# Performance work log

Hardware: AMD Instinct MI355X
Metric: run time of the kernel (lower is better)

The kernel has to match this reference:

```python
import jax, jax.numpy as jnp
import numpy as np


def setup_inputs() -> dict:
    key = jax.random.key(0)
    k1, k2, k3, k4 = jax.random.split(key, 4)
    B, Tv, Ta, D = 8, 2048, 2048, 256
    return {
        "visual_features": jax.random.normal(k1, (B, Tv, D), dtype=jnp.float32),
        "audio_features": jax.random.normal(k2, (B, Ta, D), dtype=jnp.float32),
        "visual_weights": jax.random.uniform(k3, (D, D), dtype=jnp.float32),
        "audio_weights": jax.random.uniform(k4, (D, D), dtype=jnp.float32),
        "num_neighbors": 8,
    }


def _pairwise_l2(vm, am):
    # ||v - a|| via the expanded form to avoid the [B,Tv,Ta,D] intermediate.
    sq = (
        jnp.sum(vm * vm, -1)[:, :, None]
        + jnp.sum(am * am, -1)[:, None, :]
        - 2.0 * jnp.einsum("btd,bsd->bts", vm, am)
    )
    sq = jnp.maximum(sq, 0.0)
    # safe sqrt: subgradient 0 at 0 (matches torch.norm backward convention)
    return jnp.where(sq > 0, jnp.sqrt(jnp.where(sq > 0, sq, 1.0)), 0.0)


def reference(visual_features, audio_features, visual_weights, audio_weights, num_neighbors):
    vm = visual_features @ visual_weights  # [B,Tv,D]
    am = audio_features @ audio_weights    # [B,Ta,D]
    graph = jnp.exp(-_pairwise_l2(vm, am))  # [B,Tv,Ta]
    # topk over the visual axis (dim=1): move it last for lax.top_k
    _, idx = jax.lax.top_k(jnp.swapaxes(graph, 1, 2), num_neighbors)  # [B,Ta,k]
    idx = jnp.swapaxes(idx, 1, 2)  # [B,k,Ta]
    # broadcasted gather along axis 1: result [B,k,Ta,D]
    vn = jnp.take_along_axis(visual_features[:, :, None, :], idx[..., None], axis=1)
    an = jnp.take_along_axis(audio_features[:, :, None, :], idx[..., None], axis=1)
    # mean over dim=2 (the Ta axis of the gathered neighbors) -> [B,k,D]
    return vn.mean(axis=2), an.mean(axis=2)
```

## Files before the change

### kernel.cpp

```cpp
#include <hip/hip_runtime.h>
#include <cstddef>
#include <cstdint>

namespace {
constexpr int kB   = 8;
constexpr int kT   = 2048;
constexpr int kD   = 256;
constexpr int kK   = 8;
constexpr int kM   = kB * kT;
constexpr int kNCH = 64;
constexpr int kNC  = kB * kT;
constexpr int kColCap = 64;
constexpr int kOvCap  = 1 << 17;
constexpr int kStr = 264;
constexpr float kMinNormalF = 1.17549435e-38f;
}

typedef __attribute__((ext_vector_type(8)))  __bf16 bf16x8;
typedef __attribute__((ext_vector_type(16))) float  f32x16;

__device__ inline unsigned short f2bf_rne(float x) {
  unsigned u = __float_as_uint(x);
  unsigned r = (u + 0x7FFFu + ((u >> 16) & 1u)) >> 16;
  return (unsigned short)r;
}
__device__ inline float bf2f(unsigned short h) {
  return __uint_as_float((unsigned)h << 16);
}
union FragU { uint4 u4; bf16x8 v; };

__global__ __launch_bounds__(256) void prep(const float* __restrict__ W0,
                                            const float* __restrict__ W1,
                                            unsigned short* __restrict__ T0,
                                            unsigned short* __restrict__ T1,
                                            unsigned* __restrict__ zeroBase,
                                            int zeroWords) {
  const int blk = blockIdx.x;
  if (blk < 128) {
    const float* W = (blk & 64) ? W1 : W0;
    unsigned short* WT = (blk & 64) ? T1 : T0;
    const int t = blk & 63;
    const int c0 = (t & 7) * 32, k0 = (t >> 3) * 32;
    __shared__ float tile[32][33];
    const int tx = threadIdx.x & 31, ty = threadIdx.x >> 5;
#pragma unroll
    for (int i = 0; i < 4; ++i)
      tile[ty + i * 8][tx] = W[(size_t)(k0 + ty + i * 8) * kD + c0 + tx];
    __syncthreads();
#pragma unroll
    for (int i = 0; i < 4; ++i)
      WT[(size_t)(c0 + ty + i * 8) * kD + k0 + tx] = f2bf_rne(tile[tx][ty + i * 8]);
  } else {
    for (int i = (blk - 128) * 256 + threadIdx.x; i < zeroWords; i += 32 * 256)
      zeroBase[i] = 0u;
  }
}

__global__ __launch_bounds__(256) void gemm_hyb(const float* __restrict__ Xv,
                                                const float* __restrict__ Xa,
                                                const unsigned short* __restrict__ WvT,
                                                const unsigned short* __restrict__ WaT,
                                                unsigned short* __restrict__ Cv,
                                                unsigned short* __restrict__ Ca,
                                                float* __restrict__ nv,
                                                float* __restrict__ na) {
  __shared__ unsigned short S[64 * kStr];
  const int z = blockIdx.z;
  const float* X = z ? Xa : Xv;
  const unsigned short* WT = z ? WaT : WvT;
  unsigned short* Cb = z ? Ca : Cv;
  float* nrm = z ? na : nv;
  const int r0 = blockIdx.x * 64;
  const int cHalf = blockIdx.y;
  const int tid = threadIdx.x;
  const int w = tid >> 6, lane = tid & 63;
  const int wt = w & 1, wc = w >> 1;
  const int half = lane >> 5, ln = lane & 31;

#pragma unroll
  for (int i = 0; i < 16; ++i) {
    const int idx = i * 256 + tid;
    const int row = idx >> 6, g = idx & 63;
    const float4 v = *reinterpret_cast<const float4*>(X + (size_t)(r0 + row) * kD + g * 4);
    ushort4 o;
    o.x = f2bf_rne(v.x); o.y = f2bf_rne(v.y); o.z = f2bf_rne(v.z); o.w = f2bf_rne(v.w);
    *reinterpret_cast<ushort4*>(S + row * kStr + g * 4) = o;
  }
  __syncthreads();
  uint4 afr[16];
#pragma unroll
  for (int kc = 0; kc < 16; ++kc)
    afr[kc] = *reinterpret_cast<const uint4*>(S + (wt * 32 + ln) * kStr + kc * 16 + half * 8);

  float ns[16];
#pragma unroll
  for (int r = 0; r < 16; ++r) ns[r] = 0.0f;

  for (int ct = 0; ct < 2; ++ct) {
    const int c0 = (cHalf * 2 + ct) * 64;
    __syncthreads();
#pragma unroll
    for (int i = 0; i < 8; ++i) {
      const int idx = i * 256 + tid;
      const int row = idx >> 5, g = idx & 31;
      const uint4 v = *reinterpret_cast<const uint4*>(WT + (size_t)(c0 + row) * kD + g * 8);
      *reinterpret_cast<uint4*>(S + row * kStr + g * 8) = v;
    }
    __syncthreads();
    f32x16 acc;
#pragma unroll
    for (int i = 0; i < 16; ++i) acc[i] = 0.0f;
#pragma unroll
    for (int kc = 0; kc < 16; ++kc) {
      FragU fa, fb;
      fa.u4 = afr[kc];
      fb.u4 = *reinterpret_cast<const uint4*>(S + (wc * 32 + ln) * kStr + kc * 16 + half * 8);
      acc = __builtin_amdgcn_mfma_f32_32x32x16_bf16(fa.v, fb.v, acc, 0, 0, 0);
    }
    const int col = c0 + wc * 32 + ln;
#pragma unroll
    for (int r = 0; r < 16; ++r) {
      const int row = r0 + wt * 32 + (r & 3) + 8 * (r >> 2) + 4 * half;
      const unsigned short us = f2bf_rne(acc[r]);
      Cb[(size_t)row * kD + col] = us;
      const float f = bf2f(us);
      ns[r] += f * f;
    }
  }
#pragma unroll
  for (int r = 0; r < 16; ++r) {
    float v = ns[r];
#pragma unroll
    for (int off = 1; off < 32; off <<= 1) v += __shfl_xor(v, off, 64);
    if (ln == 0) {
      const int row = r0 + wt * 32 + (r & 3) + 8 * (r >> 2) + 4 * half;
      atomicAdd(nrm + row, v);
    }
  }
}

__global__ __launch_bounds__(256) void keys_v12(const unsigned short* __restrict__ vmb,
                                                const unsigned short* __restrict__ amb,
                                                const float* __restrict__ vn2,
                                                const float* __restrict__ an2,
                                                unsigned* __restrict__ colCount,
                                                uint2* __restrict__ colRecs,
                                                unsigned* __restrict__ ovCount,
                                                uint2* __restrict__ ovRecs) {
  __shared__ unsigned short S[64 * kStr];
  const int b = blockIdx.z;
  const int t0 = blockIdx.x * 128;
  const int sr0 = blockIdx.y * 256;
  const int tid = threadIdx.x;
  const int w = tid >> 6, lane = tid & 63;
  const int half = lane >> 5, ln = lane & 31;

  uint4 afr[16];
#pragma unroll
  for (int h = 0; h < 2; ++h) {
#pragma unroll
    for (int i = 0; i < 8; ++i) {
      const int idx = i * 256 + tid;
      const int row = idx >> 5, g = idx & 31;
      const uint4 v = *reinterpret_cast<const uint4*>(
          vmb + ((size_t)b * kT + t0 + h * 64 + row) * kD + g * 8);
      *reinterpret_cast<uint4*>(S + row * kStr + g * 8) = v;
    }
    __syncthreads();
    if ((w >> 1) == h) {
#pragma unroll
      for (int kc = 0; kc < 16; ++kc)
        afr[kc] = *reinterpret_cast<const uint4*>(S + ((w & 1) * 32 + ln) * kStr + kc * 16 + half * 8);
    }
    __syncthreads();
  }

  const float* v2p = vn2 + (size_t)b * kT + t0 + w * 32;

  for (int st = 0; st < 4; ++st) {
    const int s0 = sr0 + st * 64;
    if (st) __syncthreads();
#pragma unroll
    for (int i = 0; i < 8; ++i) {
      const int idx = i * 256 + tid;
      const int row = idx >> 5, g = idx & 31;
      const uint4 v = *reinterpret_cast<const uint4*>(
          amb + ((size_t)b * kT + s0 + row) * kD + g * 8);
      *reinterpret_cast<uint4*>(S + row * kStr + g * 8) = v;
    }
    __syncthreads();
    f32x16 acc[2];
#pragma unroll
    for (int j = 0; j < 2; ++j)
#pragma unroll
      for (int i = 0; i < 16; ++i) acc[j][i] = 0.0f;
#pragma unroll
    for (int kc = 0; kc < 16; ++kc) {
      FragU fa; fa.u4 = afr[kc];
#pragma unroll
      for (int ss = 0; ss < 2; ++ss) {
        FragU fb;
        fb.u4 = *reinterpret_cast<const uint4*>(S + (ss * 32 + ln) * kStr + kc * 16 + half * 8);
        acc[ss] = __builtin_amdgcn_mfma_f32_32x32x16_bf16(fa.v, fb.v, acc[ss], 0, 0, 0);
      }
    }
#pragma unroll
    for (int ss = 0; ss < 2; ++ss) {
      const int s = s0 + ss * 32 + ln;
      const float a2 = an2[(size_t)b * kT + s];
      const int c = (b << 11) | s;
#pragma unroll
      for (int g = 0; g < 4; ++g) {
        const float4 v2 = *reinterpret_cast<const float4*>(v2p + g * 8 + half * 4);
        const float v2a[4] = {v2.x, v2.y, v2.z, v2.w};
#pragma unroll
        for (int q = 0; q < 4; ++q) {
          const float raw = v2a[q] + a2 - 2.0f * acc[ss][4 * g + q];
          if (raw < 7744.0f) {
            const float dist = sqrtf(fmaxf(raw, 0.0f));
            const float e = expf(-dist);
            if (e >= kMinNormalF) {
              const int t = t0 + w * 32 + g * 8 + half * 4 + q;
              const unsigned slot = atomicAdd(&colCount[c], 1u);
              if (slot < (unsigned)kColCap) {
                colRecs[(size_t)c * kColCap + slot] = make_uint2(__float_as_uint(e), (unsigned)t);
              } else {
                const unsigned pos = ((unsigned)b << 22) | ((unsigned)s << 11) | (unsigned)t;
                const unsigned oi = atomicAdd(ovCount, 1u);
                if (oi < (unsigned)kOvCap) ovRecs[oi] = make_uint2(__float_as_uint(e), pos);
              }
            }
          }
        }
      }
    }
  }
}

__global__ __launch_bounds__(256) void finalize_topk(const unsigned* __restrict__ colCount,
                                                     const uint2* __restrict__ colRecs,
                                                     const unsigned* __restrict__ ovCount,
                                                     const uint2* __restrict__ ovRecs,
                                                     int* __restrict__ idxT) {
  const int c = blockIdx.x * 256 + threadIdx.x;
  unsigned K[8];
  int T[8];
#pragma unroll
  for (int i = 0; i < 8; ++i) { K[i] = 0u; T[i] = 0x7FFFFFFF; }
  const int cnt = (int)colCount[c];
  const int m = min(cnt, kColCap);
  for (int i = 0; i < m; ++i) {
    const uint2 r = colRecs[(size_t)c * kColCap + i];
    const unsigned kx = r.x;
    const int tx = (int)r.y;
    if (kx > K[7] || (kx == K[7] && tx < T[7])) {
      K[7] = kx; T[7] = tx;
#pragma unroll
      for (int q = 7; q >= 1; --q) {
        const bool sw = (K[q] > K[q - 1]) || (K[q] == K[q - 1] && T[q] < T[q - 1]);
        if (sw) {
          const unsigned tk = K[q]; K[q] = K[q - 1]; K[q - 1] = tk;
          const int tt = T[q];      T[q] = T[q - 1]; T[q - 1] = tt;
        }
      }
    }
  }
  if (cnt > kColCap) {
    int n = (int)*ovCount;
    if (n > kOvCap) n = kOvCap;
    for (int i = 0; i < n; ++i) {
      const uint2 r = ovRecs[i];
      if ((int)(r.y >> 11) == c) {
        const unsigned kx = r.x;
        const int tx = (int)(r.y & 2047u);
        if (kx > K[7] || (kx == K[7] && tx < T[7])) {
          K[7] = kx; T[7] = tx;
#pragma unroll
          for (int q = 7; q >= 1; --q) {
            const bool sw = (K[q] > K[q - 1]) || (K[q] == K[q - 1] && T[q] < T[q - 1]);
            if (sw) {
              const unsigned tk = K[q]; K[q] = K[q - 1]; K[q - 1] = tk;
              const int tt = T[q];      T[q] = T[q - 1]; T[q - 1] = tt;
            }
          }
        }
      }
    }
  }
  int mcnt = 0;
#pragma unroll
  for (int i = 0; i < 8; ++i) if (K[i] > 0u) mcnt++;
  int outv[8];
#pragma unroll
  for (int i = 0; i < 8; ++i) outv[i] = T[i];
  int cand = 0;
  for (int r = mcnt; r < 8; ++r) {
    bool taken = true;
    while (taken) {
      taken = false;
#pragma unroll
      for (int q = 0; q < 8; ++q)
        if (q < mcnt && T[q] == cand) taken = true;
      if (taken) cand++;
    }
    outv[r] = cand++;
  }
  const int b = c >> 11, s = c & 2047;
#pragma unroll
  for (int r = 0; r < 8; ++r) idxT[((size_t)b * kK + r) * kT + s] = outv[r];
}

__global__ __launch_bounds__(256) void gather_kernel(const float* __restrict__ visual,
                                                     const float* __restrict__ audio,
                                                     const int* __restrict__ idxT,
                                                     float* __restrict__ pv,
                                                     float* __restrict__ pa) {
  const int blk = blockIdx.x;
  const int ch = blk & (kNCH - 1);
  const int bj = blk / kNCH;
  const int b = bj >> 3;
  const int d = threadIdx.x;
  const int* ip = idxT + (size_t)bj * kT + ch * (kT / kNCH);
  float accV = 0.f, accA = 0.f;
  for (int g = 0; g < kT / kNCH / 4; ++g) {
    const int4 cur = *reinterpret_cast<const int4*>(ip + g * 4);
    const int ts[4] = {cur.x, cur.y, cur.z, cur.w};
#pragma unroll
    for (int u = 0; u < 4; ++u) {
      const size_t base = ((size_t)b * kT + ts[u]) * kD + d;
      accV += visual[base];
      accA += audio[base];
    }
  }
  pv[(size_t)blk * kD + d] = accV;
  pa[(size_t)blk * kD + d] = accA;
}

__global__ __launch_bounds__(256) void reduce_kernel(const float* __restrict__ pv,
                                                     const float* __restrict__ pa,
                                                     float* __restrict__ out) {
  const int bj = blockIdx.x;
  const int d = threadIdx.x;
  float sV = 0.f, sA = 0.f;
#pragma unroll 8
  for (int ch = 0; ch < kNCH; ++ch) {
    sV += pv[((size_t)bj * kNCH + ch) * kD + d];
    sA += pa[((size_t)bj * kNCH + ch) * kD + d];
  }
  out[(size_t)bj * kD + d] = sV * (1.0f / kT);
  out[(size_t)kB * kK * kD + (size_t)bj * kD + d] = sA * (1.0f / kT);
}

extern "C" void kernel_launch(void* const* d_in, const int* in_sizes, int n_in,
                              void* d_out, int out_size, void* d_ws, size_t ws_size,
                              hipStream_t stream) {
  (void)in_sizes; (void)n_in; (void)out_size; (void)ws_size;
  const float* visual = (const float*)d_in[0];
  const float* audio  = (const float*)d_in[1];
  const float* Wv     = (const float*)d_in[2];
  const float* Wa     = (const float*)d_in[3];
  float* out = (float*)d_out;

  char* ws = (char*)d_ws;
  unsigned short* WvT = (unsigned short*)ws;
  unsigned short* WaT = WvT + (size_t)kD * kD;
  unsigned short* vmb = WaT + (size_t)kD * kD;
  unsigned short* amb = vmb + (size_t)kM * kD;
  float* vn2 = (float*)(amb + (size_t)kM * kD);
  float* an2 = vn2 + kM;
  unsigned* colCount = (unsigned*)(an2 + kM);
  unsigned* ovCount  = colCount + kNC;
  uint2* colRecs = (uint2*)(ovCount + 8);
  uint2* ovRecs  = colRecs + (size_t)kNC * kColCap;
  int* idxT = (int*)(ovRecs + kOvCap);
  float* pv = (float*)(idxT + (size_t)kB * kK * kT);
  float* pa = pv + (size_t)kB * kK * kNCH * kD;
  const int zeroWords = 2 * kM + kNC + 8;

  prep<<<dim3(160), 256, 0, stream>>>(Wv, Wa, WvT, WaT, (unsigned*)vn2, zeroWords);
  gemm_hyb<<<dim3(kM / 64, 2, 2), 256, 0, stream>>>(visual, audio, WvT, WaT,
                                                    vmb, amb, vn2, an2);
  keys_v12<<<dim3(kT / 128, kT / 256, kB), 256, 0, stream>>>(vmb, amb, vn2, an2,
                                                             colCount, colRecs, ovCount, ovRecs);
  finalize_topk<<<dim3(kNC / 256), 256, 0, stream>>>(colCount, colRecs, ovCount, ovRecs, idxT);
  gather_kernel<<<dim3(kB * kK * kNCH), 256, 0, stream>>>(visual, audio, idxT, pv, pa);
  reduce_kernel<<<dim3(kB * kK), 256, 0, stream>>>(pv, pa, out);
}
```

Measured before the change: 175.5 us.

## Fuse all pipeline stages into one persistent cooperative kernel with grid syncs

Adds a persistent cooperative megakernel that runs weight transpose, projection GEMM, distance/key generation, top-k finalize plus gather, and reduction as stages separated by grid.sync(). It replaces six separate kernel launches and the launch gaps between them. The grid is sized from occupancy and capped at 1024 blocks. The old multi-kernel path stays as a fallback if the cooperative launch fails. Risks include grid-sync cost, lower parallelism in the heavy stages because of the capped grid, and top-k now being fused into the gather blocks with redundant per-chunk recomputation.

```diff
diff --git a/kernel.cpp b/kernel.cpp
--- a/kernel.cpp
+++ b/kernel.cpp
@@ -1,6 +1,9 @@
 #include <hip/hip_runtime.h>
+#include <hip/hip_cooperative_groups.h>
 #include <cstddef>
 #include <cstdint>
+
+namespace cg = cooperative_groups;
 
 namespace {
 constexpr int kB   = 8;
@@ -28,6 +31,313 @@
   return __uint_as_float((unsigned)h << 16);
 }
 union FragU { uint4 u4; bf16x8 v; };
+
+__global__ __launch_bounds__(256, 2) void mega(const float* __restrict__ visual,
+                                               const float* __restrict__ audio,
+                                               const float* __restrict__ Wv,
+                                               const float* __restrict__ Wa,
+                                               float* __restrict__ out,
+                                               char* __restrict__ ws) {
+  unsigned short* WvT = (unsigned short*)ws;
+  unsigned short* WaT = WvT + (size_t)kD * kD;
+  unsigned short* vmb = WaT + (size_t)kD * kD;
+  unsigned short* amb = vmb + (size_t)kM * kD;
+  float* vn2 = (float*)(amb + (size_t)kM * kD);
+  float* an2 = vn2 + kM;
+  unsigned* colCount = (unsigned*)(an2 + kM);
+  unsigned* ovCount  = colCount + kNC;
+  uint2* colRecs = (uint2*)(ovCount + 8);
+  uint2* ovRecs  = colRecs + (size_t)kNC * kColCap;
+  float* pv = (float*)(ovRecs + kOvCap);
+  float* pa = pv + (size_t)4096 * kD;
+
+  __shared__ unsigned short S[64 * kStr];
+  cg::grid_group grid = cg::this_grid();
+  const int G = gridDim.x;
+  const int blk = blockIdx.x;
+  const int tid = threadIdx.x;
+  const int w = tid >> 6, lane = tid & 63;
+  const int half = lane >> 5, ln = lane & 31;
+
+  for (int t = blk; t < 128; t += G) {
+    __syncthreads();
+    const float* W = (t & 64) ? Wa : Wv;
+    unsigned short* WT = (t & 64) ? WaT : WvT;
+    const int tt = t & 63;
+    const int c0 = (tt & 7) * 32, k0 = (tt >> 3) * 32;
+    float* tile = (float*)S;
+    const int tx = tid & 31, ty = tid >> 5;
+#pragma unroll
+    for (int i = 0; i < 4; ++i)
+      tile[(ty + i * 8) * 33 + tx] = W[(size_t)(k0 + ty + i * 8) * kD + c0 + tx];
+    __syncthreads();
+#pragma unroll
+    for (int i = 0; i < 4; ++i)
+      WT[(size_t)(c0 + ty + i * 8) * kD + k0 + tx] = f2bf_rne(tile[tx * 33 + ty + i * 8]);
+  }
+  {
+    unsigned* zb = (unsigned*)vn2;
+    const int zeroWords = 2 * kM + kNC + 8;
+    for (int i = blk * 256 + tid; i < zeroWords; i += G * 256) zb[i] = 0u;
+  }
+  grid.sync();
+
+  for (int task = blk; task < 1024; task += G) {
+    const int z = task >> 9;
+    const int cHalf = (task >> 8) & 1;
+    const int r0 = (task & 255) * 64;
+    const float* X = z ? audio : visual;
+    const unsigned short* WT = z ? WaT : WvT;
+    unsigned short* Cb = z ? amb : vmb;
+    float* nrm = z ? an2 : vn2;
+    const int wt = w & 1, wc = w >> 1;
+
+    __syncthreads();
+#pragma unroll
+    for (int i = 0; i < 16; ++i) {
+      const int idx = i * 256 + tid;
+      const int row = idx >> 6, g = idx & 63;
+      const float4 v = *reinterpret_cast<const float4*>(X + (size_t)(r0 + row) * kD + g * 4);
+      ushort4 o;
+      o.x = f2bf_rne(v.x); o.y = f2bf_rne(v.y); o.z = f2bf_rne(v.z); o.w = f2bf_rne(v.w);
+      *reinterpret_cast<ushort4*>(S + row * kStr + g * 4) = o;
+    }
+    __syncthreads();
+    uint4 afr[16];
+#pragma unroll
+    for (int kc = 0; kc < 16; ++kc)
+      afr[kc] = *reinterpret_cast<const uint4*>(S + (wt * 32 + ln) * kStr + kc * 16 + half * 8);
+
+    float ns[16];
+#pragma unroll
+    for (int r = 0; r < 16; ++r) ns[r] = 0.0f;
+
+    for (int ct = 0; ct < 2; ++ct) {
+      const int c0 = (cHalf * 2 + ct) * 64;
+      __syncthreads();
+#pragma unroll
+      for (int i = 0; i < 8; ++i) {
+        const int idx = i * 256 + tid;
+        const int row = idx >> 5, g = idx & 31;
+        const uint4 v = *reinterpret_cast<const uint4*>(WT + (size_t)(c0 + row) * kD + g * 8);
+        *reinterpret_cast<uint4*>(S + row * kStr + g * 8) = v;
+      }
+      __syncthreads();
+      f32x16 acc;
+#pragma unroll
+      for (int i = 0; i < 16; ++i) acc[i] = 0.0f;
+#pragma unroll
+      for (int kc = 0; kc < 16; ++kc) {
+        FragU fa, fb;
+        fa.u4 = afr[kc];
+        fb.u4 = *reinterpret_cast<const uint4*>(S + (wc * 32 + ln) * kStr + kc * 16 + half * 8);
+        acc = __builtin_amdgcn_mfma_f32_32x32x16_bf16(fa.v, fb.v, acc, 0, 0, 0);
+      }
+      const int col = c0 + wc * 32 + ln;
+#pragma unroll
+      for (int r = 0; r < 16; ++r) {
+        const int row = r0 + wt * 32 + (r & 3) + 8 * (r >> 2) + 4 * half;
+        const unsigned short us = f2bf_rne(acc[r]);
+        Cb[(size_t)row * kD + col] = us;
+        const float f = bf2f(us);
+        ns[r] += f * f;
+      }
+    }
+#pragma unroll
+    for (int r = 0; r < 16; ++r) {
+      float v = ns[r];
+#pragma unroll
+      for (int off = 1; off < 32; off <<= 1) v += __shfl_xor(v, off, 64);
+      if (ln == 0) {
+        const int row = r0 + wt * 32 + (r & 3) + 8 * (r >> 2) + 4 * half;
+        atomicAdd(nrm + row, v);
+      }
+    }
+  }
+  grid.sync();
+
+  for (int task = blk; task < 1024; task += G) {
+    const int b = task >> 7;
+    const int rem = task & 127;
+    const int t0 = (rem >> 3) * 128;
+    const int sr0 = (rem & 7) * 256;
+
+    uint4 afr[16];
+#pragma unroll
+    for (int h = 0; h < 2; ++h) {
+      __syncthreads();
+#pragma unroll
+      for (int i = 0; i < 8; ++i) {
+        const int idx = i * 256 + tid;
+        const int row = idx >> 5, g = idx & 31;
+        const uint4 v = *reinterpret_cast<const uint4*>(
+            vmb + ((size_t)b * kT + t0 + h * 64 + row) * kD + g * 8);
+        *reinterpret_cast<uint4*>(S + row * kStr + g * 8) = v;
+      }
+      __syncthreads();
+      if ((w >> 1) == h) {
+#pragma unroll
+        for (int kc = 0; kc < 16; ++kc)
+          afr[kc] = *reinterpret_cast<const uint4*>(S + ((w & 1) * 32 + ln) * kStr + kc * 16 + half * 8);
+      }
+    }
+
+    const float* v2p = vn2 + (size_t)b * kT + t0 + w * 32;
+
+    for (int st = 0; st < 4; ++st) {
+      const int s0 = sr0 + st * 64;
+      __syncthreads();
+#pragma unroll
+      for (int i = 0; i < 8; ++i) {
+        const int idx = i * 256 + tid;
+        const int row = idx >> 5, g = idx & 31;
+        const uint4 v = *reinterpret_cast<const uint4*>(
+            amb + ((size_t)b * kT + s0 + row) * kD + g * 8);
+        *reinterpret_cast<uint4*>(S + row * kStr + g * 8) = v;
+      }
+      __syncthreads();
+      f32x16 acc[2];
+#pragma unroll
+      for (int j = 0; j < 2; ++j)
+#pragma unroll
+        for (int i = 0; i < 16; ++i) acc[j][i] = 0.0f;
+#pragma unroll
+      for (int kc = 0; kc < 16; ++kc) {
+        FragU fa; fa.u4 = afr[kc];
+#pragma unroll
+        for (int ss = 0; ss < 2; ++ss) {
+          FragU fb;
+          fb.u4 = *reinterpret_cast<const uint4*>(S + (ss * 32 + ln) * kStr + kc * 16 + half * 8);
+          acc[ss] = __builtin_amdgcn_mfma_f32_32x32x16_bf16(fa.v, fb.v, acc[ss], 0, 0, 0);
+        }
+      }
+#pragma unroll
+      for (int ss = 0; ss < 2; ++ss) {
+        const int s = s0 + ss * 32 + ln;
+        const float a2 = an2[(size_t)b * kT + s];
+        const int c = (b << 11) | s;
+#pragma unroll
+        for (int g = 0; g < 4; ++g) {
+          const float4 v2 = *reinterpret_cast<const float4*>(v2p + g * 8 + half * 4);
+          const float v2a[4] = {v2.x, v2.y, v2.z, v2.w};
+#pragma unroll
+          for (int q = 0; q < 4; ++q) {
+            const float raw = v2a[q] + a2 - 2.0f * acc[ss][4 * g + q];
+            if (raw < 7744.0f) {
+              const float dist = sqrtf(fmaxf(raw, 0.0f));
+              const float e = expf(-dist);
+              if (e >= kMinNormalF) {
+                const int t = t0 + w * 32 + g * 8 + half * 4 + q;
+                const unsigned slot = atomicAdd(&colCount[c], 1u);
+                if (slot < (unsigned)kColCap) {
+                  colRecs[(size_t)c * kColCap + slot] = make_uint2(__float_as_uint(e), (unsigned)t);
+                } else {
+                  const unsigned pos = ((unsigned)b << 22) | ((unsigned)s << 11) | (unsigned)t;
+                  const unsigned oi = atomicAdd(ovCount, 1u);
+                  if (oi < (unsigned)kOvCap) ovRecs[oi] = make_uint2(__float_as_uint(e), pos);
+                }
+              }
+            }
+          }
+        }
+      }
+    }
+  }
+  grid.sync();
+
+  for (int u = blk; u < 4096; u += G) {
+    const int bj = u >> 6, ch = u & 63;
+    const int b = bj >> 3, j = bj & 7;
+    int* sIdx = (int*)S;
+    __syncthreads();
+    if (tid < 32) {
+      const int s = ch * 32 + tid;
+      const int c = (b << 11) | s;
+      unsigned K[8]; int T[8];
+#pragma unroll
+      for (int i = 0; i < 8; ++i) { K[i] = 0u; T[i] = 0x7FFFFFFF; }
+      const int cnt = (int)colCount[c];
+      const int m = min(cnt, kColCap);
+      for (int i = 0; i < m; ++i) {
+        const uint2 r = colRecs[(size_t)c * kColCap + i];
+        const unsigned kx = r.x; const int tx = (int)r.y;
+        if (kx > K[7] || (kx == K[7] && tx < T[7])) {
+          K[7] = kx; T[7] = tx;
+#pragma unroll
+          for (int q = 7; q >= 1; --q) {
+            const bool sw = (K[q] > K[q - 1]) || (K[q] == K[q - 1] && T[q] < T[q - 1]);
+            if (sw) {
+              const unsigned tk = K[q]; K[q] = K[q - 1]; K[q - 1] = tk;
+              const int tt = T[q];      T[q] = T[q - 1]; T[q - 1] = tt;
+            }
+          }
+        }
+      }
+      if (cnt > kColCap) {
+        int n = (int)*ovCount;
+        if (n > kOvCap) n = kOvCap;
+        for (int i = 0; i < n; ++i) {
+          const uint2 r = ovRecs[i];
+          if ((int)(r.y >> 11) == c) {
+            const unsigned kx = r.x; const int tx = (int)(r.y & 2047u);
+            if (kx > K[7] || (kx == K[7] && tx < T[7])) {
+              K[7] = kx; T[7] = tx;
+#pragma unroll
+              for (int q = 7; q >= 1; --q) {
+                const bool sw = (K[q] > K[q - 1]) || (K[q] == K[q - 1] && T[q] < T[q - 1]);
+                if (sw) {
+                  const unsigned tk = K[q]; K[q] = K[q - 1]; K[q - 1] = tk;
+                  const int tt = T[q];      T[q] = T[q - 1]; T[q - 1] = tt;
+                }
+              }
+            }
+          }
+        }
+      }
+      int mcnt = 0;
+#pragma unroll
+      for (int i = 0; i < 8; ++i) if (K[i] > 0u) mcnt++;
+      int outv[8];
+#pragma unroll
+      for (int i = 0; i < 8; ++i) outv[i] = T[i];
+      int cand = 0;
+      for (int r = mcnt; r < 8; ++r) {
+        bool taken = true;
+        while (taken) {
+          taken = false;
+#pragma unroll
+          for (int q = 0; q < 8; ++q)
+            if (q < mcnt && T[q] == cand) taken = true;
+          if (taken) cand++;
+        }
+        outv[r] = cand++;
+      }
+      sIdx[tid] = outv[j];
+    }
+    __syncthreads();
+    float accV = 0.f, accA = 0.f;
+    for (int i = 0; i < 32; ++i) {
+      const int t = sIdx[i];
+      const size_t base = ((size_t)b * kT + t) * kD + tid;
+      accV += visual[base];
+      accA += audio[base];
+    }
+    pv[(size_t)u * kD + tid] = accV;
+    pa[(size_t)u * kD + tid] = accA;
+  }
+  grid.sync();
+
+  for (int bj = blk; bj < kB * kK; bj += G) {
+    float sV = 0.f, sA = 0.f;
+#pragma unroll 8
+    for (int ch = 0; ch < 64; ++ch) {
+      sV += pv[((size_t)bj * 64 + ch) * kD + tid];
+      sA += pa[((size_t)bj * 64 + ch) * kD + tid];
+    }
+    out[(size_t)bj * kD + tid] = sV * (1.0f / kT);
+    out[(size_t)kB * kK * kD + (size_t)bj * kD + tid] = sA * (1.0f / kT);
+  }
+}
 
 __global__ __launch_bounds__(256) void prep(const float* __restrict__ W0,
                                             const float* __restrict__ W1,
@@ -360,9 +670,9 @@
   const float* Wv     = (const float*)d_in[2];
   const float* Wa     = (const float*)d_in[3];
   float* out = (float*)d_out;
-
-  char* ws = (char*)d_ws;
-  unsigned short* WvT = (unsigned short*)ws;
+  char* wsc = (char*)d_ws;
+
+  unsigned short* WvT = (unsigned short*)wsc;
   unsigned short* WaT = WvT + (size_t)kD * kD;
   unsigned short* vmb = WaT + (size_t)kD * kD;
   unsigned short* amb = vmb + (size_t)kM * kD;
@@ -372,17 +682,37 @@
   unsigned* ovCount  = colCount + kNC;
   uint2* colRecs = (uint2*)(ovCount + 8);
   uint2* ovRecs  = colRecs + (size_t)kNC * kColCap;
-  int* idxT = (int*)(ovRecs + kOvCap);
-  float* pv = (float*)(idxT + (size_t)kB * kK * kT);
-  float* pa = pv + (size_t)kB * kK * kNCH * kD;
+  float* pv = (float*)(ovRecs + kOvCap);
+  float* pa = pv + (size_t)4096 * kD;
+  int* idxT = (int*)(pa + (size_t)4096 * kD);
   const int zeroWords = 2 * kM + kNC + 8;
 
-  prep<<<dim3(160), 256, 0, stream>>>(Wv, Wa, WvT, WaT, (unsigned*)vn2, zeroWords);
-  gemm_hyb<<<dim3(kM / 64, 2, 2), 256, 0, stream>>>(visual, audio, WvT, WaT,
-                                                    vmb, amb, vn2, an2);
-  keys_v12<<<dim3(kT / 128, kT / 256, kB), 256, 0, stream>>>(vmb, amb, vn2, an2,
-                                                             colCount, colRecs, ovCount, ovRecs);
-  finalize_topk<<<dim3(kNC / 256), 256, 0, stream>>>(colCount, colRecs, ovCount, ovRecs, idxT);
-  gather_kernel<<<dim3(kB * kK * kNCH), 256, 0, stream>>>(visual, audio, idxT, pv, pa);
-  reduce_kernel<<<dim3(kB * kK), 256, 0, stream>>>(pv, pa, out);
-}
+  int dev = 0;
+  (void)hipGetDevice(&dev);
+  int numCU = 0, maxPerCU = 0;
+  (void)hipDeviceGetAttribute(&numCU, hipDeviceAttributeMultiprocessorCount, dev);
+  hipError_t qerr = hipOccupancyMaxActiveBlocksPerMultiprocessor(&maxPerCU, mega, 256, 0);
+
+  hipError_t lerr = hipErrorUnknown;
+  if (qerr == hipSuccess && maxPerCU > 0 && numCU > 0) {
+    int grid = maxPerCU * numCU;
+    if (grid > 1024) grid = 1024;
+    if (grid >= 64) {
+      void* args[] = {(void*)&visual, (void*)&audio, (void*)&Wv, (void*)&Wa,
+                      (void*)&out, (void*)&wsc};
+      lerr = hipLaunchCooperativeKernel((const void*)mega, dim3(grid), dim3(256),
+                                        args, 0, stream);
+    }
+  }
+  if (lerr != hipSuccess) {
+    (void)hipGetLastError();
+    prep<<<dim3(160), 256, 0, stream>>>(Wv, Wa, WvT, WaT, (unsigned*)vn2, zeroWords);
+    gemm_hyb<<<dim3(kM / 64, 2, 2), 256, 0, stream>>>(visual, audio, WvT, WaT,
+                                                      vmb, amb, vn2, an2);
+    keys_v12<<<dim3(kT / 128, kT / 256, kB), 256, 0, stream>>>(vmb, amb, vn2, an2,
+                                                               colCount, colRecs, ovCount, ovRecs);
+    finalize_topk<<<dim3(kNC / 256), 256, 0, stream>>>(colCount, colRecs, ovCount, ovRecs, idxT);
+    gather_kernel<<<dim3(kB * kK * kNCH), 256, 0, stream>>>(visual, audio, idxT, pv, pa);
+    reduce_kernel<<<dim3(kB * kK), 256, 0, stream>>>(pv, pa, out);
+  }
+}
```

Measured after the change: 359.7 us. 105% more time.

## Stage GEMM tiles via async global-to-LDS loads with XOR swizzle; fuse top-k into gather

Applied to the files above, without the earlier changes.

Replaces the register round-trip tile staging in the projection GEMM and distance kernel with global_load_lds async 16-byte copies into an XOR-swizzled, unpadded LDS layout, and reads fragments through the matching swizzle. Separately merges the per-column top-k finalize into the gather kernel, so each block recomputes the top-8 for its 32 columns and keeps the indices in shared memory, removing the idxT buffer and one launch. The fused version repeats the top-k selection once per neighbor slot (8x redundant work) and runs it on only 32 threads per block, which may delay the gather loads.

```diff
diff --git a/kernel.cpp b/kernel.cpp
--- a/kernel.cpp
+++ b/kernel.cpp
@@ -8,7 +8,6 @@
 constexpr int kD   = 256;
 constexpr int kK   = 8;
 constexpr int kM   = kB * kT;
-constexpr int kNCH = 64;
 constexpr int kNC  = kB * kT;
 constexpr int kColCap = 64;
 constexpr int kOvCap  = 1 << 17;
@@ -28,6 +27,28 @@
   return __uint_as_float((unsigned)h << 16);
 }
 union FragU { uint4 u4; bf16x8 v; };
+
+__device__ inline void async16(const unsigned short* g, unsigned short* l) {
+  __builtin_amdgcn_global_load_lds(
+      (const __attribute__((address_space(1))) unsigned int*)(const void*)g,
+      (__attribute__((address_space(3))) unsigned int*)(void*)l, 16, 0, 0);
+}
+
+__device__ inline void stage_tile_async(const unsigned short* src,
+                                        unsigned short* S, int w, int lane) {
+  const int hi = lane >> 5, lo = lane & 31;
+#pragma unroll
+  for (int i = 0; i < 8; ++i) {
+    const int p = w * 8 + i;
+    const int rowl = p * 2 + hi;
+    const int c = lo ^ (rowl & 31);
+    async16(src + (size_t)rowl * kD + c * 8, S + p * 512);
+  }
+}
+__device__ inline uint4 lds_frag(const unsigned short* S, int row, int kc, int half) {
+  const int c = (kc * 2 + half) ^ (row & 31);
+  return *reinterpret_cast<const uint4*>(S + row * 256 + c * 8);
+}
 
 __global__ __launch_bounds__(256) void prep(const float* __restrict__ W0,
                                             const float* __restrict__ W1,
@@ -99,13 +120,7 @@
   for (int ct = 0; ct < 2; ++ct) {
     const int c0 = (cHalf * 2 + ct) * 64;
     __syncthreads();
-#pragma unroll
-    for (int i = 0; i < 8; ++i) {
-      const int idx = i * 256 + tid;
-      const int row = idx >> 5, g = idx & 31;
-      const uint4 v = *reinterpret_cast<const uint4*>(WT + (size_t)(c0 + row) * kD + g * 8);
-      *reinterpret_cast<uint4*>(S + row * kStr + g * 8) = v;
-    }
+    stage_tile_async(WT + (size_t)c0 * kD, S, w, lane);
     __syncthreads();
     f32x16 acc;
 #pragma unroll
@@ -114,7 +129,7 @@
     for (int kc = 0; kc < 16; ++kc) {
       FragU fa, fb;
       fa.u4 = afr[kc];
-      fb.u4 = *reinterpret_cast<const uint4*>(S + (wc * 32 + ln) * kStr + kc * 16 + half * 8);
+      fb.u4 = lds_frag(S, wc * 32 + ln, kc, half);
       acc = __builtin_amdgcn_mfma_f32_32x32x16_bf16(fa.v, fb.v, acc, 0, 0, 0);
     }
     const int col = c0 + wc * 32 + ln;
@@ -139,7 +154,7 @@
   }
 }
 
-__global__ __launch_bounds__(256) void keys_v12(const unsigned short* __restrict__ vmb,
+__global__ __launch_bounds__(256) void keys_v14(const unsigned short* __restrict__ vmb,
                                                 const unsigned short* __restrict__ amb,
                                                 const float* __restrict__ vn2,
                                                 const float* __restrict__ an2,
@@ -147,7 +162,7 @@
                                                 uint2* __restrict__ colRecs,
                                                 unsigned* __restrict__ ovCount,
                                                 uint2* __restrict__ ovRecs) {
-  __shared__ unsigned short S[64 * kStr];
+  __shared__ unsigned short S[64 * 256];
   const int b = blockIdx.z;
   const int t0 = blockIdx.x * 128;
   const int sr0 = blockIdx.y * 256;
@@ -158,36 +173,22 @@
   uint4 afr[16];
 #pragma unroll
   for (int h = 0; h < 2; ++h) {
-#pragma unroll
-    for (int i = 0; i < 8; ++i) {
-      const int idx = i * 256 + tid;
-      const int row = idx >> 5, g = idx & 31;
-      const uint4 v = *reinterpret_cast<const uint4*>(
-          vmb + ((size_t)b * kT + t0 + h * 64 + row) * kD + g * 8);
-      *reinterpret_cast<uint4*>(S + row * kStr + g * 8) = v;
-    }
+    __syncthreads();
+    stage_tile_async(vmb + ((size_t)b * kT + t0 + h * 64) * kD, S, w, lane);
     __syncthreads();
     if ((w >> 1) == h) {
 #pragma unroll
       for (int kc = 0; kc < 16; ++kc)
-        afr[kc] = *reinterpret_cast<const uint4*>(S + ((w & 1) * 32 + ln) * kStr + kc * 16 + half * 8);
-    }
-    __syncthreads();
+        afr[kc] = lds_frag(S, (w & 1) * 32 + ln, kc, half);
+    }
   }
 
   const float* v2p = vn2 + (size_t)b * kT + t0 + w * 32;
 
   for (int st = 0; st < 4; ++st) {
     const int s0 = sr0 + st * 64;
-    if (st) __syncthreads();
-#pragma unroll
-    for (int i = 0; i < 8; ++i) {
-      const int idx = i * 256 + tid;
-      const int row = idx >> 5, g = idx & 31;
-      const uint4 v = *reinterpret_cast<const uint4*>(
-          amb + ((size_t)b * kT + s0 + row) * kD + g * 8);
-      *reinterpret_cast<uint4*>(S + row * kStr + g * 8) = v;
-    }
+    __syncthreads();
+    stage_tile_async(amb + ((size_t)b * kT + s0) * kD, S, w, lane);
     __syncthreads();
     f32x16 acc[2];
 #pragma unroll
@@ -200,7 +201,7 @@
 #pragma unroll
       for (int ss = 0; ss < 2; ++ss) {
         FragU fb;
-        fb.u4 = *reinterpret_cast<const uint4*>(S + (ss * 32 + ln) * kStr + kc * 16 + half * 8);
+        fb.u4 = lds_frag(S, ss * 32 + ln, kc, half);
         acc[ss] = __builtin_amdgcn_mfma_f32_32x32x16_bf16(fa.v, fb.v, acc[ss], 0, 0, 0);
       }
     }
@@ -237,103 +238,93 @@
   }
 }
 
-__global__ __launch_bounds__(256) void finalize_topk(const unsigned* __restrict__ colCount,
-                                                     const uint2* __restrict__ colRecs,
-                                                     const unsigned* __restrict__ ovCount,
-                                                     const uint2* __restrict__ ovRecs,
-                                                     int* __restrict__ idxT) {
-  const int c = blockIdx.x * 256 + threadIdx.x;
-  unsigned K[8];
-  int T[8];
-#pragma unroll
-  for (int i = 0; i < 8; ++i) { K[i] = 0u; T[i] = 0x7FFFFFFF; }
-  const int cnt = (int)colCount[c];
-  const int m = min(cnt, kColCap);
-  for (int i = 0; i < m; ++i) {
-    const uint2 r = colRecs[(size_t)c * kColCap + i];
-    const unsigned kx = r.x;
-    const int tx = (int)r.y;
-    if (kx > K[7] || (kx == K[7] && tx < T[7])) {
-      K[7] = kx; T[7] = tx;
-#pragma unroll
-      for (int q = 7; q >= 1; --q) {
-        const bool sw = (K[q] > K[q - 1]) || (K[q] == K[q - 1] && T[q] < T[q - 1]);
-        if (sw) {
-          const unsigned tk = K[q]; K[q] = K[q - 1]; K[q - 1] = tk;
-          const int tt = T[q];      T[q] = T[q - 1]; T[q - 1] = tt;
+__global__ __launch_bounds__(256) void gather_fused(const float* __restrict__ visual,
+                                                    const float* __restrict__ audio,
+                                                    const unsigned* __restrict__ colCount,
+                                                    const uint2* __restrict__ colRecs,
+                                                    const unsigned* __restrict__ ovCount,
+                                                    const uint2* __restrict__ ovRecs,
+                                                    float* __restrict__ pv,
+                                                    float* __restrict__ pa) {
+  __shared__ int sIdx[32];
+  const int u = blockIdx.x;
+  const int bj = u >> 6, ch = u & 63;
+  const int b = bj >> 3, j = bj & 7;
+  const int tid = threadIdx.x;
+  if (tid < 32) {
+    const int s = ch * 32 + tid;
+    const int c = (b << 11) | s;
+    unsigned K[8]; int T[8];
+#pragma unroll
+    for (int i = 0; i < 8; ++i) { K[i] = 0u; T[i] = 0x7FFFFFFF; }
+    const int cnt = (int)colCount[c];
+    const int m = min(cnt, kColCap);
+    for (int i = 0; i < m; ++i) {
+      const uint2 r = colRecs[(size_t)c * kColCap + i];
+      const unsigned kx = r.x; const int tx = (int)r.y;
+      if (kx > K[7] || (kx == K[7] && tx < T[7])) {
+        K[7] = kx; T[7] = tx;
+#pragma unroll
+        for (int q = 7; q >= 1; --q) {
+          const bool sw = (K[q] > K[q - 1]) || (K[q] == K[q - 1] && T[q] < T[q - 1]);
+          if (sw) {
+            const unsigned tk = K[q]; K[q] = K[q - 1]; K[q - 1] = tk;
+            const int tt = T[q];      T[q] = T[q - 1]; T[q - 1] = tt;
+          }
         }
       }
     }
-  }
-  if (cnt > kColCap) {
-    int n = (int)*ovCount;
-    if (n > kOvCap) n = kOvCap;
-    for (int i = 0; i < n; ++i) {
-      const uint2 r = ovRecs[i];
-      if ((int)(r.y >> 11) == c) {
-        const unsigned kx = r.x;
-        const int tx = (int)(r.y & 2047u);
-        if (kx > K[7] || (kx == K[7] && tx < T[7])) {
-          K[7] = kx; T[7] = tx;
-#pragma unroll
-          for (int q = 7; q >= 1; --q) {
-            const bool sw = (K[q] > K[q - 1]) || (K[q] == K[q - 1] && T[q] < T[q - 1]);
-            if (sw) {
-              const unsigned tk = K[q]; K[q] = K[q - 1]; K[q - 1] = tk;
-              const int tt = T[q];      T[q] = T[q - 1]; T[q - 1] = tt;
+    if (cnt > kColCap) {
+      int n = (int)*ovCount;
+      if (n > kOvCap) n = kOvCap;
+      for (int i = 0; i < n; ++i) {
+        const uint2 r = ovRecs[i];
+        if ((int)(r.y >> 11) == c) {
+          const unsigned kx = r.x; const int tx = (int)(r.y & 2047u);
+          if (kx > K[7] || (kx == K[7] && tx < T[7])) {
+            K[7] = kx; T[7] = tx;
+#pragma unroll
+            for (int q = 7; q >= 1; --q) {
+              const bool sw = (K[q] > K[q - 1]) || (K[q] == K[q - 1] && T[q] < T[q - 1]);
+              if (sw) {
+                const unsigned tk = K[q]; K[q] = K[q - 1]; K[q - 1] = tk;
+                const int tt = T[q];      T[q] = T[q - 1]; T[q - 1] = tt;
+              }
             }
           }
         }
       }
     }
-  }
-  int mcnt = 0;
-#pragma unroll
-  for (int i = 0; i < 8; ++i) if (K[i] > 0u) mcnt++;
-  int outv[8];
-#pragma unroll
-  for (int i = 0; i < 8; ++i) outv[i] = T[i];
-  int cand = 0;
-  for (int r = mcnt; r < 8; ++r) {
-    bool taken = true;
-    while (taken) {
-      taken = false;
-#pragma unroll
-      for (int q = 0; q < 8; ++q)
-        if (q < mcnt && T[q] == cand) taken = true;
-      if (taken) cand++;
-    }
-    outv[r] = cand++;
-  }
-  const int b = c >> 11, s = c & 2047;
-#pragma unroll
-  for (int r = 0; r < 8; ++r) idxT[((size_t)b * kK + r) * kT + s] = outv[r];
-}
-
-__global__ __launch_bounds__(256) void gather_kernel(const float* __restrict__ visual,
-                                                     const float* __restrict__ audio,
-                                                     const int* __restrict__ idxT,
-                                                     float* __restrict__ pv,
-                                                     float* __restrict__ pa) {
-  const int blk = blockIdx.x;
-  const int ch = blk & (kNCH - 1);
-  const int bj = blk / kNCH;
-  const int b = bj >> 3;
-  const int d = threadIdx.x;
-  const int* ip = idxT + (size_t)bj * kT + ch * (kT / kNCH);
+    int mcnt = 0;
+#pragma unroll
+    for (int i = 0; i < 8; ++i) if (K[i] > 0u) mcnt++;
+    int outv[8];
+#pragma unroll
+    for (int i = 0; i < 8; ++i) outv[i] = T[i];
+    int cand = 0;
+    for (int r = mcnt; r < 8; ++r) {
+      bool taken = true;
+      while (taken) {
+        taken = false;
+#pragma unroll
+        for (int q = 0; q < 8; ++q)
+          if (q < mcnt && T[q] == cand) taken = true;
+        if (taken) cand++;
+      }
+      outv[r] = cand++;
+    }
+    sIdx[tid] = outv[j];
+  }
+  __syncthreads();
   float accV = 0.f, accA = 0.f;
-  for (int g = 0; g < kT / kNCH / 4; ++g) {
-    const int4 cur = *reinterpret_cast<const int4*>(ip + g * 4);
-    const int ts[4] = {cur.x, cur.y, cur.z, cur.w};
-#pragma unroll
-    for (int u = 0; u < 4; ++u) {
-      const size_t base = ((size_t)b * kT + ts[u]) * kD + d;
-      accV += visual[base];
-      accA += audio[base];
-    }
-  }
-  pv[(size_t)blk * kD + d] = accV;
-  pa[(size_t)blk * kD + d] = accA;
+  for (int i = 0; i < 32; ++i) {
+    const int t = sIdx[i];
+    const size_t base = ((size_t)b * kT + t) * kD + tid;
+    accV += visual[base];
+    accA += audio[base];
+  }
+  pv[(size_t)u * kD + tid] = accV;
+  pa[(size_t)u * kD + tid] = accA;
 }
 
 __global__ __launch_bounds__(256) void reduce_kernel(const float* __restrict__ pv,
@@ -343,9 +334,9 @@
   const int d = threadIdx.x;
   float sV = 0.f, sA = 0.f;
 #pragma unroll 8
-  for (int ch = 0; ch < kNCH; ++ch) {
-    sV += pv[((size_t)bj * kNCH + ch) * kD + d];
-    sA += pa[((size_t)bj * kNCH + ch) * kD + d];
+  for (int ch = 0; ch < 64; ++ch) {
+    sV += pv[((size_t)bj * 64 + ch) * kD + d];
+    sA += pa[((size_t)bj * 64 + ch) * kD + d];
   }
   out[(size_t)bj * kD + d] = sV * (1.0f / kT);
   out[(size_t)kB * kK * kD + (size_t)bj * kD + d] = sA * (1.0f / kT);
@@ -372,17 +363,16 @@
   unsigned* ovCount  = colCount + kNC;
   uint2* colRecs = (uint2*)(ovCount + 8);
   uint2* ovRecs  = colRecs + (size_t)kNC * kColCap;
-  int* idxT = (int*)(ovRecs + kOvCap);
-  float* pv = (float*)(idxT + (size_t)kB * kK * kT);
-  float* pa = pv + (size_t)kB * kK * kNCH * kD;
+  float* pv = (float*)(ovRecs + kOvCap);
+  float* pa = pv + (size_t)4096 * kD;
   const int zeroWords = 2 * kM + kNC + 8;
 
   prep<<<dim3(160), 256, 0, stream>>>(Wv, Wa, WvT, WaT, (unsigned*)vn2, zeroWords);
   gemm_hyb<<<dim3(kM / 64, 2, 2), 256, 0, stream>>>(visual, audio, WvT, WaT,
                                                     vmb, amb, vn2, an2);
-  keys_v12<<<dim3(kT / 128, kT / 256, kB), 256, 0, stream>>>(vmb, amb, vn2, an2,
+  keys_v14<<<dim3(kT / 128, kT / 256, kB), 256, 0, stream>>>(vmb, amb, vn2, an2,
                                                              colCount, colRecs, ovCount, ovRecs);
-  finalize_topk<<<dim3(kNC / 256), 256, 0, stream>>>(colCount, colRecs, ovCount, ovRecs, idxT);
-  gather_kernel<<<dim3(kB * kK * kNCH), 256, 0, stream>>>(visual, audio, idxT, pv, pa);
+  gather_fused<<<dim3(4096), 256, 0, stream>>>(visual, audio, colCount, colRecs,
+                                               ovCount, ovRecs, pv, pa);
   reduce_kernel<<<dim3(kB * kK), 256, 0, stream>>>(pv, pa, out);
 }
```

After: 158.6 us. 1.11x faster.
